# Kernel optimization log

Measured on AMD Instinct MI355X. Metric: run time of the kernel, lower is better.

The kernel has to match this reference:

```python
import jax, jax.numpy as jnp
import numpy as np

N = 8192
D_IN = 1024
D_OUT = 1024


def setup_inputs() -> dict:
    key = jax.random.key(0)
    k1, k2, k3, k4 = jax.random.split(key, 4)
    # param scales mimic reset_parameters: weight ~ U(-r, r), transfers ~ N(0, 0.001)
    r = np.sqrt(6.0 / (D_IN + D_OUT))
    x = jax.random.normal(k1, (N, D_IN), dtype=jnp.float32)
    weight = jax.random.uniform(k2, (D_IN, D_OUT), dtype=jnp.float32, minval=-r, maxval=r)
    transferi = jax.random.normal(k3, (D_IN, D_IN), dtype=jnp.float32) * 0.001
    transferj = jax.random.normal(k4, (D_IN, D_IN), dtype=jnp.float32) * 0.001
    return {"x": x, "weight": weight, "transferi": transferi, "transferj": transferj}


def reference(x, weight, transferi, transferj):
    # support = x @ W  -> [N, out]
    support = x @ weight
    # NOTE: the original torch code uses transferi for BOTH projections (transferj unused)
    x_i = x @ transferi            # [N, in]
    x_j = x @ transferi            # [N, in]
    scores = x_i @ x_j.T           # [N, N] inner-product attention, no scaling
    attn = jax.nn.softmax(scores, axis=1)
    return attn @ support          # [N, out]
```

## Files before the change

### kernel.cpp

```cpp
#include <hip/hip_runtime.h>
#include <hip/hip_bf16.h>
#include <cstddef>

#define NQ 8192
#define DD 1024

typedef __attribute__((ext_vector_type(8))) short s8v;
typedef __attribute__((ext_vector_type(8))) int i8v;
typedef __attribute__((ext_vector_type(4))) float f32x4;
typedef __attribute__((ext_vector_type(16))) float f32x16;

typedef const __attribute__((address_space(1))) unsigned int* gptr_t;
typedef __attribute__((address_space(3))) unsigned int* lptr_t;

#define SCALE_1_16 0x7B7B7B7Bu

__device__ inline unsigned short f2bf(float f) {
  union { float f; unsigned u; } v; v.f = f;
  unsigned r = (v.u + 0x7FFFu + ((v.u >> 16) & 1u)) >> 16;
  return (unsigned short)r;
}
__device__ inline float bits2f(unsigned u) {
  union { unsigned u; float f; } v; v.u = u;
  return v.f;
}

__device__ inline unsigned char f2e4m3(float x) {
  union { float f; unsigned u; } v; v.f = x;
  const unsigned s = (v.u >> 31) << 7;
  unsigned au = v.u & 0x7FFFFFFFu;
  if (au > 0x43E00000u) au = 0x43E00000u;
  if (au >= 0x3C800000u) {
    const unsigned rounded = au + 0x7FFFFu + ((au >> 20) & 1u);
    const unsigned e8 = ((rounded >> 23) & 0xFF) - 120u;
    const unsigned m8 = (rounded >> 20) & 7u;
    return (unsigned char)(s | (e8 << 3) | m8);
  } else {
    union { unsigned u; float f; } a; a.u = au;
    const unsigned q = (unsigned)rintf(a.f * 512.0f);
    return (unsigned char)(s | q);
  }
}

__device__ inline i8v make_i8v(int4 a, int4 b) {
  i8v v;
  v[0] = a.x; v[1] = a.y; v[2] = a.z; v[3] = a.w;
  v[4] = b.x; v[5] = b.y; v[6] = b.z; v[7] = b.w;
  return v;
}

template <int KDIM, int ASTR, int BSTR>
__device__ inline void mfma_core_db(const unsigned short* __restrict__ A,
                                    const unsigned short* __restrict__ B,
                                    int i0, int j0, int tid,
                                    unsigned short* __restrict__ As0,
                                    unsigned short* __restrict__ As1,
                                    unsigned short* __restrict__ Bs0,
                                    unsigned short* __restrict__ Bs1,
                                    f32x4 (&acc)[4][4]) {
  const int lane = tid & 63;
  const int w = tid >> 6;
  const int wr = (w >> 1) * 64;
  const int wc = (w & 1) * 64;
  const int l16 = lane & 15;
  const int lq = lane >> 4;
  const int srow = lane >> 3;
  const int scol = (((lane & 7) ^ (srow & 7)) * 8);

  auto stage = [&](unsigned short* dA, unsigned short* dB, int kk) {
#pragma unroll
    for (int t = 0; t < 4; t++) {
      const int r0 = w * 32 + t * 8;
      const unsigned short* g = &A[(size_t)(i0 + r0 + srow) * ASTR + kk + scol];
      __builtin_amdgcn_global_load_lds((gptr_t)(const void*)g,
                                       (lptr_t)(void*)&dA[r0 * 64], 16, 0, 0);
    }
#pragma unroll
    for (int t = 0; t < 4; t++) {
      const int r0 = w * 32 + t * 8;
      const unsigned short* g = &B[(size_t)(j0 + r0 + srow) * BSTR + kk + scol];
      __builtin_amdgcn_global_load_lds((gptr_t)(const void*)g,
                                       (lptr_t)(void*)&dB[r0 * 64], 16, 0, 0);
    }
  };

  stage(As0, Bs0, 0);
  asm volatile("s_waitcnt vmcnt(0)" ::: "memory");
  __syncthreads();

  const int h = l16 & 7;
  unsigned short* curA = As0;
  unsigned short* curB = Bs0;
  unsigned short* nxtA = As1;
  unsigned short* nxtB = Bs1;
#pragma unroll 1
  for (int t = 0; t < KDIM / 64; t++) {
    if (t < KDIM / 64 - 1) stage(nxtA, nxtB, (t + 1) * 64);
    s8v af[4][2], bf[4][2];
#pragma unroll
    for (int q = 0; q < 4; q++)
#pragma unroll
      for (int s = 0; s < 2; s++) {
        const int ch = ((s * 4 + lq) ^ h) * 8;
        af[q][s] = *(const s8v*)&curA[(wr + 16 * q + l16) * 64 + ch];
        bf[q][s] = *(const s8v*)&curB[(wc + 16 * q + l16) * 64 + ch];
      }
#pragma unroll
    for (int s = 0; s < 2; s++)
#pragma unroll
      for (int a = 0; a < 4; a++)
#pragma unroll
        for (int b = 0; b < 4; b++)
          acc[a][b] = __builtin_amdgcn_mfma_f32_16x16x32_bf16(
              af[a][s], bf[b][s], acc[a][b], 0, 0, 0);
    asm volatile("s_waitcnt vmcnt(0)" ::: "memory");
    __syncthreads();
    unsigned short* tA = curA; curA = nxtA; nxtA = tA;
    unsigned short* tB = curB; curB = nxtB; nxtB = tB;
  }
}

__global__ void f32_to_bf16(const float* __restrict__ in,
                            unsigned short* __restrict__ out, int n4) {
  int i = (blockIdx.x * blockDim.x + threadIdx.x);
  if (i < n4) {
    const float4 v = *(const float4*)&in[i * 4];
    ushort4 o;
    o.x = f2bf(v.x); o.y = f2bf(v.y); o.z = f2bf(v.z); o.w = f2bf(v.w);
    *(ushort4*)&out[i * 4] = o;
  }
}

__global__ void zero_f32(float* __restrict__ p, int n) {
  const int i = blockIdx.x * blockDim.x + threadIdx.x;
  if (i < n) p[i] = 0.f;
}

__global__ void transpose_cvt(const float* __restrict__ in,
                              unsigned short* __restrict__ out, int R, int C) {
  __shared__ float t[32][33];
  const int bx = blockIdx.x;
  const int by = blockIdx.y;
  const int x = threadIdx.x & 31;
  const int y = threadIdx.x >> 5;
#pragma unroll
  for (int i = 0; i < 32; i += 8)
    t[y + i][x] = in[(size_t)(by * 32 + y + i) * C + bx * 32 + x];
  __syncthreads();
#pragma unroll
  for (int i = 0; i < 32; i += 8)
    out[(size_t)(bx * 32 + y + i) * R + by * 32 + x] = f2bf(t[x][y + i]);
}

template <int NST, bool FP8OUT>
__global__ __launch_bounds__(256, 2)
void proj_gemm(const unsigned short* __restrict__ A,
               const unsigned short* __restrict__ BT,
               void* __restrict__ Cout) {
  __shared__ __align__(16) unsigned short As[2][128 * 64];
  __shared__ __align__(16) unsigned short Bs[2][128 * 64];
  const int tid = threadIdx.x;
  const int m0 = blockIdx.y * 128;
  const int n0 = blockIdx.x * 128;

  f32x4 acc[4][4];
#pragma unroll
  for (int a = 0; a < 4; a++)
#pragma unroll
    for (int b = 0; b < 4; b++) acc[a][b] = (f32x4){0.f, 0.f, 0.f, 0.f};

  mfma_core_db<DD, DD, DD>(A, BT, m0, n0, tid, As[0], As[1], Bs[0], Bs[1], acc);

  const int lane = tid & 63;
  const int w = tid >> 6;
  const int wr = (w >> 1) * 64, wc = (w & 1) * 64;
  const int l16 = lane & 15, lq = lane >> 4;
#pragma unroll
  for (int ti = 0; ti < 4; ti++)
#pragma unroll
    for (int r = 0; r < 4; r++) {
      const int row = m0 + wr + 16 * ti + lq * 4 + r;
#pragma unroll
      for (int tj = 0; tj < 4; tj++) {
        const int col = n0 + wc + 16 * tj + l16;
        if (FP8OUT) {
          ((unsigned char*)Cout)[(size_t)row * NST + col] =
              f2e4m3(acc[ti][tj][r] * 16.f);
        } else {
          ((unsigned short*)Cout)[(size_t)row * NST + col] = f2bf(acc[ti][tj][r]);
        }
      }
    }
}

__global__ __launch_bounds__(256, 3)
void qk_fp8(const unsigned char* __restrict__ xif,
            unsigned short* __restrict__ P,
            float* __restrict__ lsum) {
  __shared__ __align__(16) unsigned char smem[128 * 65 * 4];
  unsigned char* AsF0 = smem;
  unsigned char* BsF0 = smem + 8192;
  unsigned char* AsF1 = smem + 16384;
  unsigned char* BsF1 = smem + 24576;
  const int tid = threadIdx.x;
  const int lane = tid & 63;
  const int w = tid >> 6;
  const int i0 = blockIdx.y * 128;
  const int j0 = blockIdx.x * 128;

  f32x16 acc[2][2];
#pragma unroll
  for (int a = 0; a < 2; a++)
#pragma unroll
    for (int b = 0; b < 2; b++)
#pragma unroll
      for (int r = 0; r < 16; r++) acc[a][b][r] = 0.f;

  const int srow = lane >> 2;
  const int slot = lane & 3;
  const int kb = lane >> 5;
  const int l31 = lane & 31;

  auto stage = [&](unsigned char* dA, unsigned char* dB, int kk) {
#pragma unroll
    for (int t = 0; t < 2; t++) {
      const int r = w * 32 + t * 16 + srow;
      const int c = slot ^ ((r >> 1) & 3);
      const unsigned char* ga = &xif[(size_t)(i0 + r) * DD + kk + c * 16];
      const unsigned char* gb = &xif[(size_t)(j0 + r) * DD + kk + c * 16];
      __builtin_amdgcn_global_load_lds((gptr_t)(const void*)ga,
                                       (lptr_t)(void*)&dA[(w * 32 + t * 16) * 64],
                                       16, 0, 0);
      __builtin_amdgcn_global_load_lds((gptr_t)(const void*)gb,
                                       (lptr_t)(void*)&dB[(w * 32 + t * 16) * 64],
                                       16, 0, 0);
    }
  };

  stage(AsF0, BsF0, 0);
  asm volatile("s_waitcnt vmcnt(0)" ::: "memory");
  __syncthreads();

  unsigned char* curA = AsF0;
  unsigned char* curB = BsF0;
  unsigned char* nxtA = AsF1;
  unsigned char* nxtB = BsF1;
#pragma unroll 1
  for (int t = 0; t < DD / 64; t++) {
    if (t < DD / 64 - 1) stage(nxtA, nxtB, (t + 1) * 64);

    i8v af[2], bf[2];
#pragma unroll
    for (int mi = 0; mi < 2; mi++) {
      const int ar = (w >> 1) * 64 + mi * 32 + l31;
      const int sw = (ar >> 1) & 3;
      const int4 q0 = *(const int4*)&curA[ar * 64 + ((2 * kb + 0) ^ sw) * 16];
      const int4 q1 = *(const int4*)&curA[ar * 64 + ((2 * kb + 1) ^ sw) * 16];
      af[mi] = make_i8v(q0, q1);
    }
#pragma unroll
    for (int nj = 0; nj < 2; nj++) {
      const int br = (w & 1) * 64 + nj * 32 + l31;
      const int sw = (br >> 1) & 3;
      const int4 q0 = *(const int4*)&curB[br * 64 + ((2 * kb + 0) ^ sw) * 16];
      const int4 q1 = *(const int4*)&curB[br * 64 + ((2 * kb + 1) ^ sw) * 16];
      bf[nj] = make_i8v(q0, q1);
    }
#pragma unroll
    for (int mi = 0; mi < 2; mi++)
#pragma unroll
      for (int nj = 0; nj < 2; nj++)
        acc[mi][nj] = __builtin_amdgcn_mfma_scale_f32_32x32x64_f8f6f4(
            af[mi], bf[nj], acc[mi][nj], 0 , 0 ,
            0, SCALE_1_16, 0, SCALE_1_16);

    asm volatile("s_waitcnt vmcnt(0)" ::: "memory");
    __syncthreads();
    unsigned char* tA = curA; curA = nxtA; nxtA = tA;
    unsigned char* tB = curB; curB = nxtB; nxtB = tB;
  }

  float ex0[2][16], ex1[2][16];
#pragma unroll
  for (int mi = 0; mi < 2; mi++)
#pragma unroll
    for (int reg = 0; reg < 16; reg++) {
      ex0[mi][reg] = __expf(acc[mi][0][reg]);
      ex1[mi][reg] = __expf(acc[mi][1][reg]);
    }

  const int mbase = (w >> 1) * 64;
  const int nbase = (w & 1) * 64;
  const int rowoff = 4 * (lane >> 5);
  const int cslot = (w & 1) * 32 + l31;

  float (*lsums)[65] = (float (*)[65])smem;
#pragma unroll
  for (int mi = 0; mi < 2; mi++)
#pragma unroll
    for (int r4 = 0; r4 < 4; r4++)
#pragma unroll
      for (int rr = 0; rr < 4; rr++) {
        const int reg = r4 * 4 + rr;
        const int rl = mbase + mi * 32 + rr + 8 * r4 + rowoff;
        lsums[rl][cslot] = ex0[mi][reg] + ex1[mi][reg];
      }
  __syncthreads();
  if (tid < 128) {
    float s = 0.f;
#pragma unroll
    for (int c = 0; c < 64; c++) s += lsums[tid][c];
    atomicAdd(&lsum[i0 + tid], s);
  }
  __syncthreads();

  unsigned short* tile = (unsigned short*)smem;
#pragma unroll
  for (int mi = 0; mi < 2; mi++)
#pragma unroll
    for (int r4 = 0; r4 < 4; r4++)
#pragma unroll
      for (int rr = 0; rr < 4; rr++) {
        const int reg = r4 * 4 + rr;
        const int rl = mbase + mi * 32 + rr + 8 * r4 + rowoff;
        tile[rl * 128 + nbase + l31]      = f2bf(ex0[mi][reg]);
        tile[rl * 128 + nbase + l31 + 32] = f2bf(ex1[mi][reg]);
      }
  __syncthreads();
  {
    const int rr2 = tid >> 4;
    const int ch = (tid & 15) * 8;
#pragma unroll
    for (int q = 0; q < 8; q++) {
      const int row = rr2 + q * 16;
      const int4 v = *(const int4*)&tile[row * 128 + ch];
      *(int4*)&P[(size_t)(i0 + row) * NQ + j0 + ch] = v;
    }
  }
}

__global__ __launch_bounds__(256, 2)
void pv(const unsigned short* __restrict__ P,
        const unsigned short* __restrict__ supT,
        const float* __restrict__ lsum,
        float* __restrict__ out) {
  __shared__ __align__(16) unsigned short As[2][128 * 64];
  __shared__ __align__(16) unsigned short Bs[2][128 * 64];
  const int tid = threadIdx.x;
  const int i0 = blockIdx.x * 128;
  const int n0 = blockIdx.y * 128;

  f32x4 acc[4][4];
#pragma unroll
  for (int a = 0; a < 4; a++)
#pragma unroll
    for (int b = 0; b < 4; b++) acc[a][b] = (f32x4){0.f, 0.f, 0.f, 0.f};

  mfma_core_db<NQ, NQ, NQ>(P, supT, i0, n0, tid, As[0], As[1], Bs[0], Bs[1],
                           acc);

  const int lane = tid & 63;
  const int w = tid >> 6;
  const int wr = (w >> 1) * 64, wc = (w & 1) * 64;
  const int l16 = lane & 15, lq = lane >> 4;
#pragma unroll
  for (int ti = 0; ti < 4; ti++) {
#pragma unroll
    for (int r = 0; r < 4; r++) {
      const int row = i0 + wr + 16 * ti + lq * 4 + r;
      const float linv = 1.f / lsum[row];
#pragma unroll
      for (int tj = 0; tj < 4; tj++) {
        const int col = n0 + wc + 16 * tj + l16;
        out[(size_t)row * DD + col] = acc[ti][tj][r] * linv;
      }
    }
  }
}

#define BM 64
#define BN 64
#define BK 16

__global__ __launch_bounds__(256, 4)
void gemm64(const float* __restrict__ A, const float* __restrict__ B,
            float* __restrict__ C, int M, int N, int K) {
  __shared__ __align__(16) float As[BK][BM + 4];
  __shared__ __align__(16) float Bs[BK][BN + 4];
  const int tid = threadIdx.x;
  const int tx = tid & 15;
  const int ty = tid >> 4;
  const int row0 = blockIdx.y * BM;
  const int col0 = blockIdx.x * BN;
  float acc[4][4] = {};
  for (int k0 = 0; k0 < K; k0 += BK) {
    {
      const int r = tid >> 2;
      const int c4 = (tid & 3) * 4;
      const float4 v = *(const float4*)&A[(size_t)(row0 + r) * K + k0 + c4];
      As[c4 + 0][r] = v.x; As[c4 + 1][r] = v.y;
      As[c4 + 2][r] = v.z; As[c4 + 3][r] = v.w;
    }
    {
      const int r = tid >> 4;
      const int c4 = (tid & 15) * 4;
      *(float4*)&Bs[r][c4] = *(const float4*)&B[(size_t)(k0 + r) * N + col0 + c4];
    }
    __syncthreads();
#pragma unroll
    for (int k = 0; k < BK; k++) {
      const float4 a = *(const float4*)&As[k][4 * ty];
      const float4 b = *(const float4*)&Bs[k][4 * tx];
      const float av[4] = {a.x, a.y, a.z, a.w};
      const float bv[4] = {b.x, b.y, b.z, b.w};
#pragma unroll
      for (int i = 0; i < 4; i++)
#pragma unroll
        for (int j = 0; j < 4; j++)
          acc[i][j] += av[i] * bv[j];
    }
    __syncthreads();
  }
#pragma unroll
  for (int i = 0; i < 4; i++) {
    float4 o = {acc[i][0], acc[i][1], acc[i][2], acc[i][3]};
    *(float4*)&C[(size_t)(row0 + 4 * ty + i) * N + col0 + 4 * tx] = o;
  }
}

#define IT 32
#define JT 128
#define KC 32
#define CC 128
#define NCH (DD / CC)

__global__ __launch_bounds__(256, 1)
void fused_attn(const float* __restrict__ xi, const float* __restrict__ sup,
                float* __restrict__ out) {
  __shared__ __align__(16) float XiI[KC][IT + 4];
  __shared__ __align__(16) float XiJ[KC][JT + 4];
  __shared__ __align__(16) float Ps[JT][IT + 4];
  __shared__ __align__(16) float Vs[JT][CC + 4];
  __shared__ float lsum[IT];
  const int tid = threadIdx.x;
  const int i0 = blockIdx.x * IT;
  const int ry = tid >> 5;
  const int cx = tid & 31;
  if (tid < IT) lsum[tid] = 0.f;
  float oacc[NCH][4][4];
#pragma unroll
  for (int ch = 0; ch < NCH; ch++)
#pragma unroll
    for (int i = 0; i < 4; i++)
#pragma unroll
      for (int j = 0; j < 4; j++) oacc[ch][i][j] = 0.f;
  for (int j0 = 0; j0 < NQ; j0 += JT) {
    float sacc[4][4] = {};
    for (int kc = 0; kc < DD; kc += KC) {
      __syncthreads();
      {
        const int r = tid >> 3;
        const int k4 = (tid & 7) * 4;
        const float4 v = *(const float4*)&xi[(size_t)(i0 + r) * DD + kc + k4];
        XiI[k4 + 0][r] = v.x; XiI[k4 + 1][r] = v.y;
        XiI[k4 + 2][r] = v.z; XiI[k4 + 3][r] = v.w;
      }
#pragma unroll
      for (int i = 0; i < 4; i++) {
        const int idx = tid + i * 256;
        const int r = idx >> 3;
        const int k4 = (idx & 7) * 4;
        const float4 v = *(const float4*)&xi[(size_t)(j0 + r) * DD + kc + k4];
        XiJ[k4 + 0][r] = v.x; XiJ[k4 + 1][r] = v.y;
        XiJ[k4 + 2][r] = v.z; XiJ[k4 + 3][r] = v.w;
      }
      __syncthreads();
#pragma unroll
      for (int k = 0; k < KC; k++) {
        const float4 a = *(const float4*)&XiI[k][4 * ry];
        const float4 b = *(const float4*)&XiJ[k][4 * cx];
        const float av[4] = {a.x, a.y, a.z, a.w};
        const float bv[4] = {b.x, b.y, b.z, b.w};
#pragma unroll
        for (int i = 0; i < 4; i++)
#pragma unroll
          for (int j = 0; j < 4; j++)
            sacc[i][j] += av[i] * bv[j];
      }
    }
    __syncthreads();
    float rsv[4] = {0.f, 0.f, 0.f, 0.f};
#pragma unroll
    for (int i = 0; i < 4; i++)
#pragma unroll
      for (int j = 0; j < 4; j++) {
        const float p = __expf(sacc[i][j]);
        Ps[4 * cx + j][4 * ry + i] = p;
        rsv[i] += p;
      }
#pragma unroll
    for (int m = 16; m >= 1; m >>= 1)
#pragma unroll
      for (int i = 0; i < 4; i++) rsv[i] += __shfl_xor(rsv[i], m);
    if (cx == 0) {
#pragma unroll
      for (int i = 0; i < 4; i++) lsum[4 * ry + i] += rsv[i];
    }
    for (int ch = 0; ch < NCH; ch++) {
      __syncthreads();
#pragma unroll
      for (int i = 0; i < 16; i++) {
        const int idx = tid + i * 256;
        const int r = idx >> 5;
        const int c4 = (idx & 31) * 4;
        *(float4*)&Vs[r][c4] =
            *(const float4*)&sup[(size_t)(j0 + r) * DD + ch * CC + c4];
      }
      __syncthreads();
#pragma unroll 4
      for (int jp = 0; jp < JT; jp++) {
        const float4 p = *(const float4*)&Ps[jp][4 * ry];
        const float4 v = *(const float4*)&Vs[jp][4 * cx];
        const float pvv[4] = {p.x, p.y, p.z, p.w};
        const float vv[4] = {v.x, v.y, v.z, v.w};
#pragma unroll
        for (int i = 0; i < 4; i++)
#pragma unroll
          for (int j = 0; j < 4; j++)
            oacc[ch][i][j] += pvv[i] * vv[j];
      }
    }
  }
  __syncthreads();
  float linv[4];
#pragma unroll
  for (int i = 0; i < 4; i++) linv[i] = 1.f / lsum[4 * ry + i];
#pragma unroll
  for (int ch = 0; ch < NCH; ch++)
#pragma unroll
    for (int i = 0; i < 4; i++) {
      float4 o = {oacc[ch][i][0] * linv[i], oacc[ch][i][1] * linv[i],
                  oacc[ch][i][2] * linv[i], oacc[ch][i][3] * linv[i]};
      *(float4*)&out[(size_t)(i0 + 4 * ry + i) * DD + ch * CC + 4 * cx] = o;
    }
}

extern "C" void kernel_launch(void* const* d_in, const int* in_sizes, int n_in,
                              void* d_out, int out_size, void* d_ws, size_t ws_size,
                              hipStream_t stream) {
  const float* x  = (const float*)d_in[0];
  const float* wt = (const float*)d_in[1];
  const float* ti = (const float*)d_in[2];
  float* out = (float*)d_out;

  char* ws = (char*)d_ws;
  const size_t MB = 1024 * 1024;
  const size_t NEED = 152 * MB + NQ * sizeof(float);

  if (ws_size >= NEED) {
    unsigned short* P    = (unsigned short*)ws;
    unsigned char*  xif  = (unsigned char*)(ws + 128 * MB);
    unsigned short* supT = (unsigned short*)(ws + 136 * MB);
    float* lsum          = (float*)(ws + 152 * MB);
    unsigned short* xb   = (unsigned short*)ws;
    unsigned short* tiT  = (unsigned short*)(ws + 16 * MB);
    unsigned short* wT   = (unsigned short*)(ws + 18 * MB);

    const int n4 = NQ * DD / 4;
    zero_f32<<<NQ / 256, 256, 0, stream>>>(lsum, NQ);
    f32_to_bf16<<<(n4 + 255) / 256, 256, 0, stream>>>(x, xb, n4);
    transpose_cvt<<<dim3(32, 32), 256, 0, stream>>>(ti, tiT, DD, DD);
    transpose_cvt<<<dim3(32, 32), 256, 0, stream>>>(wt, wT, DD, DD);

    proj_gemm<DD, true><<<dim3(DD / 128, NQ / 128), 256, 0, stream>>>(xb, tiT, xif);
    proj_gemm<NQ, false><<<dim3(NQ / 128, DD / 128), 256, 0, stream>>>(wT, xb, supT);

    qk_fp8<<<dim3(NQ / 128, NQ / 128), 256, 0, stream>>>(xif, P, lsum);
    pv<<<dim3(NQ / 128, DD / 128), 256, 0, stream>>>(P, supT, lsum, out);
  } else {
    float* xi32  = (float*)ws;
    float* sup32 = (float*)(ws + 32 * MB);
    dim3 ggrid(DD / BN, NQ / BM);
    gemm64<<<ggrid, 256, 0, stream>>>(x, ti, xi32, NQ, DD, DD);
    gemm64<<<ggrid, 256, 0, stream>>>(x, wt, sup32, NQ, DD, DD);
    fused_attn<<<NQ / IT, 256, 0, stream>>>(xi32, sup32, out);
  }
}
```

Measured before the change: 355.7 us.

## Widen QK fp8 tile to 128x256 per block for more operand reuse

New measurement: 364.1 us. 1.02x slower.

```diff
diff --git a/kernel.cpp b/kernel.cpp
--- a/kernel.cpp
+++ b/kernel.cpp
@@ -193,26 +193,26 @@
     }
 }
 
-__global__ __launch_bounds__(256, 3)
+__global__ __launch_bounds__(256, 2)
 void qk_fp8(const unsigned char* __restrict__ xif,
             unsigned short* __restrict__ P,
             float* __restrict__ lsum) {
-  __shared__ __align__(16) unsigned char smem[128 * 65 * 4];
-  unsigned char* AsF0 = smem;
-  unsigned char* BsF0 = smem + 8192;
-  unsigned char* AsF1 = smem + 16384;
-  unsigned char* BsF1 = smem + 24576;
+  __shared__ __align__(16) unsigned char smem[49152];
+  unsigned char* A0 = smem;
+  unsigned char* B0 = smem + 8192;
+  unsigned char* A1 = smem + 24576;
+  unsigned char* B1 = smem + 32768;
   const int tid = threadIdx.x;
   const int lane = tid & 63;
   const int w = tid >> 6;
   const int i0 = blockIdx.y * 128;
-  const int j0 = blockIdx.x * 128;
-
-  f32x16 acc[2][2];
+  const int j0 = blockIdx.x * 256;
+
+  f32x16 acc[2][4];
 #pragma unroll
   for (int a = 0; a < 2; a++)
 #pragma unroll
-    for (int b = 0; b < 2; b++)
+    for (int b = 0; b < 4; b++)
 #pragma unroll
       for (int r = 0; r < 16; r++) acc[a][b][r] = 0.f;
 
@@ -227,29 +227,34 @@
       const int r = w * 32 + t * 16 + srow;
       const int c = slot ^ ((r >> 1) & 3);
       const unsigned char* ga = &xif[(size_t)(i0 + r) * DD + kk + c * 16];
-      const unsigned char* gb = &xif[(size_t)(j0 + r) * DD + kk + c * 16];
       __builtin_amdgcn_global_load_lds((gptr_t)(const void*)ga,
                                        (lptr_t)(void*)&dA[(w * 32 + t * 16) * 64],
                                        16, 0, 0);
+    }
+#pragma unroll
+    for (int t = 0; t < 4; t++) {
+      const int r = w * 64 + t * 16 + srow;
+      const int c = slot ^ ((r >> 1) & 3);
+      const unsigned char* gb = &xif[(size_t)(j0 + r) * DD + kk + c * 16];
       __builtin_amdgcn_global_load_lds((gptr_t)(const void*)gb,
-                                       (lptr_t)(void*)&dB[(w * 32 + t * 16) * 64],
+                                       (lptr_t)(void*)&dB[(w * 64 + t * 16) * 64],
                                        16, 0, 0);
     }
   };
 
-  stage(AsF0, BsF0, 0);
+  stage(A0, B0, 0);
   asm volatile("s_waitcnt vmcnt(0)" ::: "memory");
   __syncthreads();
 
-  unsigned char* curA = AsF0;
-  unsigned char* curB = BsF0;
-  unsigned char* nxtA = AsF1;
-  unsigned char* nxtB = BsF1;
+  unsigned char* curA = A0;
+  unsigned char* curB = B0;
+  unsigned char* nxtA = A1;
+  unsigned char* nxtB = B1;
 #pragma unroll 1
   for (int t = 0; t < DD / 64; t++) {
     if (t < DD / 64 - 1) stage(nxtA, nxtB, (t + 1) * 64);
 
-    i8v af[2], bf[2];
+    i8v af[2], bf[4];
 #pragma unroll
     for (int mi = 0; mi < 2; mi++) {
       const int ar = (w >> 1) * 64 + mi * 32 + l31;
@@ -259,8 +264,8 @@
       af[mi] = make_i8v(q0, q1);
     }
 #pragma unroll
-    for (int nj = 0; nj < 2; nj++) {
-      const int br = (w & 1) * 64 + nj * 32 + l31;
+    for (int nj = 0; nj < 4; nj++) {
+      const int br = (w & 1) * 128 + nj * 32 + l31;
       const int sw = (br >> 1) & 3;
       const int4 q0 = *(const int4*)&curB[br * 64 + ((2 * kb + 0) ^ sw) * 16];
       const int4 q1 = *(const int4*)&curB[br * 64 + ((2 * kb + 1) ^ sw) * 16];
@@ -269,7 +274,7 @@
 #pragma unroll
     for (int mi = 0; mi < 2; mi++)
 #pragma unroll
-      for (int nj = 0; nj < 2; nj++)
+      for (int nj = 0; nj < 4; nj++)
         acc[mi][nj] = __builtin_amdgcn_mfma_scale_f32_32x32x64_f8f6f4(
             af[mi], bf[nj], acc[mi][nj], 0 , 0 ,
             0, SCALE_1_16, 0, SCALE_1_16);
@@ -280,17 +285,7 @@
     unsigned char* tB = curB; curB = nxtB; nxtB = tB;
   }
 
-  float ex0[2][16], ex1[2][16];
-#pragma unroll
-  for (int mi = 0; mi < 2; mi++)
-#pragma unroll
-    for (int reg = 0; reg < 16; reg++) {
-      ex0[mi][reg] = __expf(acc[mi][0][reg]);
-      ex1[mi][reg] = __expf(acc[mi][1][reg]);
-    }
-
   const int mbase = (w >> 1) * 64;
-  const int nbase = (w & 1) * 64;
   const int rowoff = 4 * (lane >> 5);
   const int cslot = (w & 1) * 32 + l31;
 
@@ -303,7 +298,10 @@
       for (int rr = 0; rr < 4; rr++) {
         const int reg = r4 * 4 + rr;
         const int rl = mbase + mi * 32 + rr + 8 * r4 + rowoff;
-        lsums[rl][cslot] = ex0[mi][reg] + ex1[mi][reg];
+        float s = 0.f;
+#pragma unroll
+        for (int nj = 0; nj < 4; nj++) s += __expf(acc[mi][nj][reg]);
+        lsums[rl][cslot] = s;
       }
   __syncthreads();
   if (tid < 128) {
@@ -315,27 +313,34 @@
   __syncthreads();
 
   unsigned short* tile = (unsigned short*)smem;
-#pragma unroll
-  for (int mi = 0; mi < 2; mi++)
-#pragma unroll
-    for (int r4 = 0; r4 < 4; r4++)
-#pragma unroll
-      for (int rr = 0; rr < 4; rr++) {
-        const int reg = r4 * 4 + rr;
-        const int rl = mbase + mi * 32 + rr + 8 * r4 + rowoff;
-        tile[rl * 128 + nbase + l31]      = f2bf(ex0[mi][reg]);
-        tile[rl * 128 + nbase + l31 + 32] = f2bf(ex1[mi][reg]);
-      }
-  __syncthreads();
-  {
-    const int rr2 = tid >> 4;
-    const int ch = (tid & 15) * 8;
-#pragma unroll
-    for (int q = 0; q < 8; q++) {
-      const int row = rr2 + q * 16;
-      const int4 v = *(const int4*)&tile[row * 128 + ch];
-      *(int4*)&P[(size_t)(i0 + row) * NQ + j0 + ch] = v;
-    }
+#pragma unroll 1
+  for (int hh = 0; hh < 2; hh++) {
+    if ((w & 1) == hh) {
+#pragma unroll
+      for (int mi = 0; mi < 2; mi++)
+#pragma unroll
+        for (int r4 = 0; r4 < 4; r4++)
+#pragma unroll
+          for (int rr = 0; rr < 4; rr++) {
+            const int reg = r4 * 4 + rr;
+            const int rl = mbase + mi * 32 + rr + 8 * r4 + rowoff;
+#pragma unroll
+            for (int nj = 0; nj < 4; nj++)
+              tile[rl * 128 + nj * 32 + l31] = f2bf(__expf(acc[mi][nj][reg]));
+          }
+    }
+    __syncthreads();
+    {
+      const int rr2 = tid >> 4;
+      const int ch = (tid & 15) * 8;
+#pragma unroll
+      for (int q = 0; q < 8; q++) {
+        const int row = rr2 + q * 16;
+        const int4 v = *(const int4*)&tile[row * 128 + ch];
+        *(int4*)&P[(size_t)(i0 + row) * NQ + j0 + hh * 128 + ch] = v;
+      }
+    }
+    __syncthreads();
   }
 }
 
@@ -575,7 +580,7 @@
     proj_gemm<DD, true><<<dim3(DD / 128, NQ / 128), 256, 0, stream>>>(xb, tiT, xif);
     proj_gemm<NQ, false><<<dim3(NQ / 128, DD / 128), 256, 0, stream>>>(wT, xb, supT);
 
-    qk_fp8<<<dim3(NQ / 128, NQ / 128), 256, 0, stream>>>(xif, P, lsum);
+    qk_fp8<<<dim3(NQ / 256, NQ / 128), 256, 0, stream>>>(xif, P, lsum);
     pv<<<dim3(NQ / 128, DD / 128), 256, 0, stream>>>(P, supT, lsum, out);
   } else {
     float* xi32  = (float*)ws;
```
